# Optimization experiments

Hardware: AMD Instinct MI355X
Metric: run time of the kernel (lower is better)

## Reference

```python
import jax, jax.numpy as jnp
import numpy as np

N_NODES = 100000
N_EDGES = 1600000
HEADS = 8
CH = 16
NEG_SLOPE = 0.2


def setup_inputs() -> dict:
    key = jax.random.key(0)
    ks = jax.random.split(key, 8)
    x = jax.random.normal(ks[0], (N_NODES, 16), dtype=jnp.float32)
    edge_index = jax.random.randint(ks[1], (2, N_EDGES), 0, N_NODES, dtype=jnp.int64)
    W = jax.random.normal(ks[2], (16, HEADS * CH), dtype=jnp.float32) * 0.25
    att_src = jax.random.normal(ks[3], (HEADS, CH), dtype=jnp.float32) * 0.25
    att_dst = jax.random.normal(ks[4], (HEADS, CH), dtype=jnp.float32) * 0.25
    bias = jax.random.normal(ks[5], (HEADS * CH,), dtype=jnp.float32) * 0.1
    fc_w = jax.random.normal(ks[6], (HEADS * CH, 5), dtype=jnp.float32) * 0.1
    fc_b = jax.random.normal(ks[7], (5,), dtype=jnp.float32) * 0.1
    return {"x": x, "edge_index": edge_index, "W": W, "att_src": att_src,
            "att_dst": att_dst, "bias": bias, "fc_w": fc_w, "fc_b": fc_b}


def reference(x, edge_index, W, att_src, att_dst, bias, fc_w, fc_b):
    N = x.shape[0]
    # PyG GATConv default: add self loops
    loops = jnp.arange(N, dtype=edge_index.dtype)
    src = jnp.concatenate([edge_index[0], loops])
    dst = jnp.concatenate([edge_index[1], loops])

    h = (x @ W).reshape(N, HEADS, CH)                 # [N,H,C]
    a_src = jnp.einsum('nhc,hc->nh', h, att_src)      # [N,H]
    a_dst = jnp.einsum('nhc,hc->nh', h, att_dst)      # [N,H]

    e = a_src[src] + a_dst[dst]                       # [E,H]
    e = jax.nn.leaky_relu(e, NEG_SLOPE)
    # segment softmax over edges grouped by destination node
    e_max = jax.ops.segment_max(e, dst, num_segments=N)
    e_exp = jnp.exp(e - e_max[dst])
    denom = jax.ops.segment_sum(e_exp, dst, num_segments=N)
    alpha = e_exp / (denom[dst] + 1e-16)              # [E,H]

    msg = alpha[:, :, None] * h[src]                  # [E,H,C]
    out = jax.ops.segment_sum(msg, dst, num_segments=N)  # [N,H,C]
    out = out.reshape(N, HEADS * CH) + bias           # concat heads + bias

    out = jax.nn.relu(out)
    # dropout is identity in eval mode
    logits = out @ fc_w + fc_b                        # [N,5]
    return jax.nn.log_softmax(logits, axis=1)
```

## Files before the change

kernel.cpp:

```cpp
#include <hip/hip_runtime.h>
#include <hip/hip_bf16.h>
#include <hip/hip_fp16.h>
#include <math.h>

#define N_NODES 100000
#define N_EDGES 1600000
#define HEADS 8
#define HC 128
#define LOG2E 1.44269504f

#define DPB 64
#define NB 1563
#define NBP (NB + 1)
#define NCH 512
#define EPC (N_EDGES / NCH)
#define CAPS 1664
#define WSTR (CAPS + 4)
#define NA 196

__global__ __launch_bounds__(512) void k_prep(
    const float* __restrict__ x, const float* __restrict__ W,
    const float* __restrict__ att_s, const float* __restrict__ att_d,
    const int* __restrict__ ei,
    unsigned short* __restrict__ a_srcb, float* __restrict__ a_dst,
    uint4* __restrict__ x2b,
    int* __restrict__ offs, unsigned* __restrict__ stg) {
    __shared__ int smem[2048 + EPC];
    __shared__ int ws8[8];
    int t = threadIdx.x;
    if (blockIdx.x >= NCH) {
        float* sM = (float*)smem;
        if (t < 256) {
            int k = t >> 4, h2 = t & 15;
            const float* av = (h2 < 8) ? att_s : att_d;
            int h = h2 & 7;
            float s = 0.f;
#pragma unroll
            for (int c = 0; c < 16; ++c)
                s = fmaf(W[k * HC + h * 16 + c], av[h * 16 + c], s);
            sM[k * 16 + h2] = s * LOG2E;
        }
        __syncthreads();
        int node = (blockIdx.x - NCH) * 512 + t;
        if (node < N_NODES) {
            const float4* xr = (const float4*)(x + node * 16);
            float4 x0 = xr[0], x1 = xr[1], x2 = xr[2], x3 = xr[3];
            float xv[16] = {x0.x, x0.y, x0.z, x0.w, x1.x, x1.y, x1.z, x1.w,
                            x2.x, x2.y, x2.z, x2.w, x3.x, x3.y, x3.z, x3.w};
            union { uint4 u[2]; __hip_bfloat162 b[8]; } px;
#pragma unroll
            for (int k = 0; k < 8; ++k)
                px.b[k] = __float22bfloat162_rn(float2{xv[2 * k], xv[2 * k + 1]});
            x2b[node * 2] = px.u[0];
            x2b[node * 2 + 1] = px.u[1];
            float oo[16];
#pragma unroll
            for (int h2 = 0; h2 < 16; ++h2) {
                float o = 0.f;
#pragma unroll
                for (int k = 0; k < 16; ++k) o = fmaf(xv[k], sM[k * 16 + h2], o);
                oo[h2] = o;
            }
            union { uint4 u; unsigned short s[8]; } pb;
#pragma unroll
            for (int h = 0; h < 8; ++h)
                pb.s[h] = __bfloat16_as_ushort(__float2bfloat16(oo[h]));
            *(uint4*)(a_srcb + (size_t)node * 8) = pb.u;
            float4 d0 = {oo[8], oo[9], oo[10], oo[11]};
            float4 d1 = {oo[12], oo[13], oo[14], oo[15]};
            *(float4*)(a_dst + (size_t)node * 8) = d0;
            *(float4*)(a_dst + (size_t)node * 8 + 4) = d1;
        }
    } else {
        int* hist = smem;
        unsigned* entries = (unsigned*)(smem + 2048);
        int c = blockIdx.x;
        hist[t] = 0; hist[t + 512] = 0; hist[t + 1024] = 0; hist[t + 1536] = 0;
        __syncthreads();
        int beg = c * EPC, end = beg + EPC;
        for (int e = beg + t; e < end; e += 512)
            atomicAdd(&hist[ei[N_EDGES + e] >> 6], 1);
        __syncthreads();
        int i0 = 4 * t;
        int v0 = hist[i0], v1 = hist[i0 + 1], v2 = hist[i0 + 2], v3 = hist[i0 + 3];
        int s1 = v0 + v1, s2 = s1 + v2, T = s2 + v3;
        int lane = t & 63, wv = t >> 6;
        int inc = T;
#pragma unroll
        for (int off = 1; off < 64; off <<= 1) {
            int y = __shfl_up(inc, off);
            if (lane >= off) inc += y;
        }
        if (lane == 63) ws8[wv] = inc;
        __syncthreads();
        int wbase = 0;
        for (int k = 0; k < wv; ++k) wbase += ws8[k];
        int e0 = wbase + inc - T;
        hist[i0] = e0; hist[i0 + 1] = e0 + v0;
        hist[i0 + 2] = e0 + s1; hist[i0 + 3] = e0 + s2;
        __syncthreads();
        int row = c * NBP;
        for (int b = t; b < NB; b += 512) offs[row + b] = hist[b];
        if (t == 0) offs[row + NB] = EPC;
        __syncthreads();
        for (int e = beg + t; e < end; e += 512) {
            int src = ei[e], dst = ei[N_EDGES + e];
            int pos = atomicAdd(&hist[dst >> 6], 1);
            entries[pos] = ((unsigned)(dst & 63) << 17) | (unsigned)src;
        }
        __syncthreads();
        unsigned* so = stg + beg;
        for (int i = t; i < EPC; i += 512) so[i] = entries[i];
    }
}

__global__ __launch_bounds__(256) void k_tr(const int* __restrict__ offs,
                                            int* __restrict__ offsT) {
    __shared__ int tile[64][65];
    int b0 = (blockIdx.x >> 3) * 64;
    int c0 = (blockIdx.x & 7) * 64;
    int t = threadIdx.x;
    for (int i = t; i < 4096; i += 256) {
        int cc = i >> 6, bb = i & 63;
        int b = b0 + bb;
        tile[bb][cc] = (b < NBP) ? offs[(c0 + cc) * NBP + b] : 0;
    }
    __syncthreads();
    for (int i = t; i < 4096; i += 256) {
        int bb = i >> 6, cc = i & 63;
        int b = b0 + bb;
        if (b < NBP) offsT[b * NCH + c0 + cc] = tile[bb][cc];
    }
}

__global__ __launch_bounds__(512) void k_gather(
    const __hip_bfloat162* __restrict__ x2b,
    const unsigned short* __restrict__ a_srcb, const float* __restrict__ W,
    const float* __restrict__ a_dst,
    const int* __restrict__ offsT, const unsigned* __restrict__ stg,
    const float* __restrict__ bias, const float* __restrict__ fc_w,
    const float* __restrict__ fc_b, float* __restrict__ out) {
    __shared__ __align__(16) unsigned buf0[(8 * WSTR) / 2];
    __shared__ __align__(16) int sbuf[CAPS];
    __shared__ __align__(16) float sW[16 * HC];
    __shared__ __align__(16) float sad[8 * DPB + 8];
    __shared__ int hist[DPB];
    __shared__ int bs[DPB + 1];
    __shared__ int rord[DPB];
    __shared__ int ws8[8];
    unsigned* estage = buf0;
    unsigned short* wst = (unsigned short*)buf0;
    int* cstage = sbuf;
    int* o0_s = sbuf;
    int* myb_s = sbuf + 512;
    int b = blockIdx.x, t = threadIdx.x;
    int d0 = b * DPB;
    for (int i = t; i < 16 * HC; i += 512) {
        int c = i & 127, k = i >> 7;
        int blk = c >> 3;
        int sb = blk ^ ((blk >> 2) & 3);
        sW[k * HC + sb * 8 + (c & 7)] = W[i];
    }
    sad[t] = (d0 * 8 + t < N_NODES * 8) ? a_dst[(size_t)d0 * 8 + t] : 0.f;
    if (t < 8) sad[8 * DPB + t] = -100000.f;
    int lane = t & 63, wv = t >> 6;
    {
        int o0 = offsT[b * NCH + t];
        int len = offsT[(b + 1) * NCH + t] - o0;
        o0_s[t] = o0;
        int inc = len;
#pragma unroll
        for (int off = 1; off < 64; off <<= 1) {
            int y = __shfl_up(inc, off);
            if (lane >= off) inc += y;
        }
        if (lane == 63) ws8[wv] = inc;
        __syncthreads();
        int wbase = 0;
        for (int k = 0; k < wv; ++k) wbase += ws8[k];
        myb_s[t] = wbase + inc - len;
        if (t == 511) myb_s[NCH] = wbase + inc;
    }
    if (t < DPB) hist[t] = (d0 + t < N_NODES) ? 1 : 0;
    __syncthreads();
    int tot = myb_s[NCH];
    for (int i = t; i < tot; i += 512) {
        int lo = 0, hi = NCH - 1;
#pragma unroll
        for (int s = 0; s < 9; ++s) {
            int mid = (lo + hi + 1) >> 1;
            if (myb_s[mid] <= i) lo = mid; else hi = mid - 1;
        }
        estage[i] = stg[lo * EPC + o0_s[lo] + (i - myb_s[lo])];
    }
    __syncthreads();
    for (int i = t; i < tot; i += 512) atomicAdd(&hist[estage[i] >> 17], 1);
    __syncthreads();
    if (t < 64) {
        int gd = d0 + t;
        bool val = gd < N_NODES;
        int len = hist[t];
        int plen = (len + 3) & ~3;
        int iv = plen;
#pragma unroll
        for (int off = 1; off < 64; off <<= 1) {
            int y = __shfl_up(iv, off);
            if (t >= off) iv += y;
        }
        int excl = iv - plen;
        bs[t] = excl;
        if (t == 63) bs[64] = iv;
        if (val) cstage[excl] = (t << 17) | gd;
        hist[t] = excl + (val ? 1 : 0);
        for (int k = len; k < plen; ++k) cstage[excl + k] = (64 << 17);
        int key = (plen << 6) | t;
#pragma unroll
        for (int k = 2; k <= 64; k <<= 1) {
#pragma unroll
            for (int jj = k >> 1; jj >= 1; jj >>= 1) {
                int partner = __shfl_xor(key, jj);
                bool up = ((t & k) == 0);
                bool takeMax = (((t & jj) != 0) == up);
                key = takeMax ? (key > partner ? key : partner)
                              : (key < partner ? key : partner);
            }
        }
        rord[t] = key & 63;
    }
    __syncthreads();
    for (int i = t; i < tot; i += 512) {
        unsigned u = estage[i];
        int pos = atomicAdd(&hist[u >> 17], 1);
        cstage[pos] = (int)u;
    }
    __syncthreads();
    int ctot = bs[DPB];
    for (int i = t; i < ctot; i += 512) {
        unsigned u = (unsigned)cstage[i];
        int s = (int)(u & 0x1FFFF);
        int dl = (int)(u >> 17);
        union { uint4 v; __hip_bfloat162 b2[4]; } pa;
        pa.v = *(const uint4*)(a_srcb + (size_t)s * 8);
        const float* adp = sad + dl * 8;
        float4 ad0 = *(const float4*)(adp);
        float4 ad1 = *(const float4*)(adp + 4);
        float2 s01 = __bfloat1622float2(pa.b2[0]);
        float2 s23 = __bfloat1622float2(pa.b2[1]);
        float2 s45 = __bfloat1622float2(pa.b2[2]);
        float2 s67 = __bfloat1622float2(pa.b2[3]);
        float e[8] = {s01.x + ad0.x, s01.y + ad0.y, s23.x + ad0.z, s23.y + ad0.w,
                      s45.x + ad1.x, s45.y + ad1.y, s67.x + ad1.z, s67.y + ad1.w};
#pragma unroll
        for (int h = 0; h < 8; ++h) {
            float eh = fmaxf(e[h], 0.2f * e[h]);
            float w = exp2f(eh);
            wst[h * WSTR + i] = __half_as_ushort(__float2half(w));
        }
    }
    __syncthreads();
    int q = t & 15, g = t >> 4;
    int head = q >> 1, i8 = q & 1;
    int c0 = head * 16 + i8 * 8;
    int blk0 = c0 >> 3;
    int sw0 = (blk0 ^ ((blk0 >> 2) & 3)) * 8;
    const unsigned short* wrow = wst + head * WSTR;
    int xofs = i8 * 16;
    const char* xb = (const char*)x2b;
    float bb[8], fwv[8][5], fbv[5];
#pragma unroll
    for (int m = 0; m < 8; ++m) bb[m] = bias[c0 + m];
#pragma unroll
    for (int m = 0; m < 8; ++m)
#pragma unroll
        for (int jj = 0; jj < 5; ++jj) fwv[m][jj] = fc_w[(c0 + m) * 5 + jj];
#pragma unroll
    for (int jj = 0; jj < 5; ++jj) fbv[jj] = fc_b[jj];
    for (int l4 = 0; l4 < 2; ++l4) {
        int l = rord[l4 == 0 ? g : 63 - g];
        int gd = d0 + l;
        if (gd >= N_NODES) continue;
        int beg = bs[l], end = bs[l + 1];
        float A[8] = {0.f, 0.f, 0.f, 0.f, 0.f, 0.f, 0.f, 0.f};
        float wsum = 0.f;
        auto acc = [&](const uint4& xv, float w) {
            union { uint4 v; __hip_bfloat162 b2[4]; } xx; xx.v = xv;
            float2 f0 = __bfloat1622float2(xx.b2[0]);
            float2 f1 = __bfloat1622float2(xx.b2[1]);
            float2 f2 = __bfloat1622float2(xx.b2[2]);
            float2 f3 = __bfloat1622float2(xx.b2[3]);
            A[0] = fmaf(w, f0.x, A[0]); A[1] = fmaf(w, f0.y, A[1]);
            A[2] = fmaf(w, f1.x, A[2]); A[3] = fmaf(w, f1.y, A[3]);
            A[4] = fmaf(w, f2.x, A[4]); A[5] = fmaf(w, f2.y, A[5]);
            A[6] = fmaf(w, f3.x, A[6]); A[7] = fmaf(w, f3.y, A[7]);
        };
        for (int j = beg; j < end; j += 4) {
            int4 cs = *(const int4*)(cstage + j);
            uint2 wu = *(const uint2*)(wrow + j);
            union { uint2 u2; __half2 h2[2]; } wq; wq.u2 = wu;
            float2 w01 = __half22float2(wq.h2[0]);
            float2 w23 = __half22float2(wq.h2[1]);
            int s0 = cs.x & 0x1FFFF, s1 = cs.y & 0x1FFFF;
            int s2 = cs.z & 0x1FFFF, s3 = cs.w & 0x1FFFF;
            uint4 xv0 = *(const uint4*)(xb + ((s0 << 5) + xofs));
            uint4 xv1 = *(const uint4*)(xb + ((s1 << 5) + xofs));
            uint4 xv2 = *(const uint4*)(xb + ((s2 << 5) + xofs));
            uint4 xv3 = *(const uint4*)(xb + ((s3 << 5) + xofs));
            acc(xv0, w01.x); acc(xv1, w01.y);
            acc(xv2, w23.x); acc(xv3, w23.y);
            wsum += (w01.x + w01.y) + (w23.x + w23.y);
        }
        float inv = 1.f / (wsum + 1e-16f);
#pragma unroll
        for (int m = 0; m < 8; ++m) A[m] *= inv;
        float ov[8] = {0.f, 0.f, 0.f, 0.f, 0.f, 0.f, 0.f, 0.f};
#pragma unroll
        for (int m = 0; m < 8; ++m) {
            float a = A[m];
            float ap = __shfl_xor(A[m], 1);
            const float* w0r = sW + (i8 * 8 + m) * HC + sw0;
            const float* w1r = sW + ((1 - i8) * 8 + m) * HC + sw0;
#pragma unroll
            for (int o = 0; o < 8; ++o) ov[o] = fmaf(a, w0r[o], ov[o]);
#pragma unroll
            for (int o = 0; o < 8; ++o) ov[o] = fmaf(ap, w1r[o], ov[o]);
        }
#pragma unroll
        for (int m = 0; m < 8; ++m) ov[m] = fmaxf(ov[m] + bb[m], 0.f);
        float p[5];
#pragma unroll
        for (int jj = 0; jj < 5; ++jj) {
            float sacc = 0.f;
#pragma unroll
            for (int m = 0; m < 8; ++m) sacc = fmaf(ov[m], fwv[m][jj], sacc);
            p[jj] = sacc;
        }
#pragma unroll
        for (int off = 8; off >= 1; off >>= 1)
#pragma unroll
            for (int jj = 0; jj < 5; ++jj) p[jj] += __shfl_xor(p[jj], off);
        if (q == 0) {
            float lg[5], mx = -1e30f;
#pragma unroll
            for (int jj = 0; jj < 5; ++jj) {
                lg[jj] = p[jj] + fbv[jj];
                mx = fmaxf(mx, lg[jj]);
            }
            float sum = 0.f;
#pragma unroll
            for (int jj = 0; jj < 5; ++jj) sum += __expf(lg[jj] - mx);
            float ls = mx + __logf(sum);
#pragma unroll
            for (int jj = 0; jj < 5; ++jj) out[gd * 5 + jj] = lg[jj] - ls;
        }
    }
}

extern "C" void kernel_launch(void* const* d_in, const int* in_sizes, int n_in,
                              void* d_out, int out_size, void* d_ws, size_t ws_size,
                              hipStream_t stream) {
    const float* x     = (const float*)d_in[0];
    const int*   ei    = (const int*)d_in[1];
    const float* W     = (const float*)d_in[2];
    const float* att_s = (const float*)d_in[3];
    const float* att_d = (const float*)d_in[4];
    const float* bias  = (const float*)d_in[5];
    const float* fc_w  = (const float*)d_in[6];
    const float* fc_b  = (const float*)d_in[7];
    float* out = (float*)d_out;

    char* ws = (char*)d_ws;
    size_t off = 0;
    auto carve = [&](size_t bytes) {
        void* p = ws + off;
        off = (off + bytes + 255) & ~(size_t)255;
        return p;
    };
    unsigned short* a_srcb = (unsigned short*)carve((size_t)N_NODES * HEADS * 2);
    float*    a_dst = (float*)   carve((size_t)N_NODES * HEADS * 4);
    uint4*    x2b   = (uint4*)   carve((size_t)N_NODES * 32);
    int*      offs  = (int*)     carve((size_t)NCH * NBP * 4);
    int*      offsT = (int*)     carve((size_t)NBP * NCH * 4);
    unsigned* stg   = (unsigned*)carve((size_t)N_EDGES * 4);

    k_prep<<<NCH + NA, 512, 0, stream>>>(x, W, att_s, att_d, ei,
                                         a_srcb, a_dst, x2b, offs, stg);
    k_tr<<<200, 256, 0, stream>>>(offs, offsT);
    k_gather<<<NB, 512, 0, stream>>>((const __hip_bfloat162*)x2b, a_srcb, W,
                                     a_dst, offsT, stg, bias, fc_w, fc_b, out);
}
```

Baseline: 169.2 us.

## Split prep kernel, fuse histogram into staging loop, drop bitonic row ordering

The combined prep kernel is split into a counting-sort kernel and a separate per-node attention-projection kernel launched with 256-thread blocks. In the gather kernel, the destination histogram is now counted in the same loop that stages edges, which removes one pass and one barrier. The bitonic sort that ordered destination rows by length for load balancing is removed, and rows are assigned to groups in a fixed interleaved order. This trades possible load imbalance across row groups for less setup work, and adds one extra kernel launch.

```diff
diff --git a/kernel.cpp b/kernel.cpp
--- a/kernel.cpp
+++ b/kernel.cpp
@@ -16,101 +16,102 @@
 #define EPC (N_EDGES / NCH)
 #define CAPS 1664
 #define WSTR (CAPS + 4)
-#define NA 196
-
-__global__ __launch_bounds__(512) void k_prep(
+#define NAB 391
+
+__global__ __launch_bounds__(512) void k_csort(
+    const int* __restrict__ ei, int* __restrict__ offs,
+    unsigned* __restrict__ stg) {
+    __shared__ int hist[2048];
+    __shared__ int entries_s[EPC];
+    __shared__ int ws8[8];
+    unsigned* entries = (unsigned*)entries_s;
+    int t = threadIdx.x;
+    int c = blockIdx.x;
+    hist[t] = 0; hist[t + 512] = 0; hist[t + 1024] = 0; hist[t + 1536] = 0;
+    __syncthreads();
+    int beg = c * EPC, end = beg + EPC;
+    for (int e = beg + t; e < end; e += 512)
+        atomicAdd(&hist[ei[N_EDGES + e] >> 6], 1);
+    __syncthreads();
+    int i0 = 4 * t;
+    int v0 = hist[i0], v1 = hist[i0 + 1], v2 = hist[i0 + 2], v3 = hist[i0 + 3];
+    int s1 = v0 + v1, s2 = s1 + v2, T = s2 + v3;
+    int lane = t & 63, wv = t >> 6;
+    int inc = T;
+#pragma unroll
+    for (int off = 1; off < 64; off <<= 1) {
+        int y = __shfl_up(inc, off);
+        if (lane >= off) inc += y;
+    }
+    if (lane == 63) ws8[wv] = inc;
+    __syncthreads();
+    int wbase = 0;
+    for (int k = 0; k < wv; ++k) wbase += ws8[k];
+    int e0 = wbase + inc - T;
+    hist[i0] = e0; hist[i0 + 1] = e0 + v0;
+    hist[i0 + 2] = e0 + s1; hist[i0 + 3] = e0 + s2;
+    __syncthreads();
+    int row = c * NBP;
+    for (int b = t; b < NB; b += 512) offs[row + b] = hist[b];
+    if (t == 0) offs[row + NB] = EPC;
+    __syncthreads();
+    for (int e = beg + t; e < end; e += 512) {
+        int src = ei[e], dst = ei[N_EDGES + e];
+        int pos = atomicAdd(&hist[dst >> 6], 1);
+        entries[pos] = ((unsigned)(dst & 63) << 17) | (unsigned)src;
+    }
+    __syncthreads();
+    unsigned* so = stg + beg;
+    for (int i = t; i < EPC; i += 512) so[i] = entries[i];
+}
+
+__global__ __launch_bounds__(256) void k_amat(
     const float* __restrict__ x, const float* __restrict__ W,
     const float* __restrict__ att_s, const float* __restrict__ att_d,
-    const int* __restrict__ ei,
     unsigned short* __restrict__ a_srcb, float* __restrict__ a_dst,
-    uint4* __restrict__ x2b,
-    int* __restrict__ offs, unsigned* __restrict__ stg) {
-    __shared__ int smem[2048 + EPC];
-    __shared__ int ws8[8];
+    uint4* __restrict__ x2b) {
+    __shared__ float sM[256];
     int t = threadIdx.x;
-    if (blockIdx.x >= NCH) {
-        float* sM = (float*)smem;
-        if (t < 256) {
-            int k = t >> 4, h2 = t & 15;
-            const float* av = (h2 < 8) ? att_s : att_d;
-            int h = h2 & 7;
-            float s = 0.f;
-#pragma unroll
-            for (int c = 0; c < 16; ++c)
-                s = fmaf(W[k * HC + h * 16 + c], av[h * 16 + c], s);
-            sM[k * 16 + h2] = s * LOG2E;
-        }
-        __syncthreads();
-        int node = (blockIdx.x - NCH) * 512 + t;
-        if (node < N_NODES) {
-            const float4* xr = (const float4*)(x + node * 16);
-            float4 x0 = xr[0], x1 = xr[1], x2 = xr[2], x3 = xr[3];
-            float xv[16] = {x0.x, x0.y, x0.z, x0.w, x1.x, x1.y, x1.z, x1.w,
-                            x2.x, x2.y, x2.z, x2.w, x3.x, x3.y, x3.z, x3.w};
-            union { uint4 u[2]; __hip_bfloat162 b[8]; } px;
-#pragma unroll
-            for (int k = 0; k < 8; ++k)
-                px.b[k] = __float22bfloat162_rn(float2{xv[2 * k], xv[2 * k + 1]});
-            x2b[node * 2] = px.u[0];
-            x2b[node * 2 + 1] = px.u[1];
-            float oo[16];
-#pragma unroll
-            for (int h2 = 0; h2 < 16; ++h2) {
-                float o = 0.f;
-#pragma unroll
-                for (int k = 0; k < 16; ++k) o = fmaf(xv[k], sM[k * 16 + h2], o);
-                oo[h2] = o;
-            }
-            union { uint4 u; unsigned short s[8]; } pb;
-#pragma unroll
-            for (int h = 0; h < 8; ++h)
-                pb.s[h] = __bfloat16_as_ushort(__float2bfloat16(oo[h]));
-            *(uint4*)(a_srcb + (size_t)node * 8) = pb.u;
-            float4 d0 = {oo[8], oo[9], oo[10], oo[11]};
-            float4 d1 = {oo[12], oo[13], oo[14], oo[15]};
-            *(float4*)(a_dst + (size_t)node * 8) = d0;
-            *(float4*)(a_dst + (size_t)node * 8 + 4) = d1;
-        }
-    } else {
-        int* hist = smem;
-        unsigned* entries = (unsigned*)(smem + 2048);
-        int c = blockIdx.x;
-        hist[t] = 0; hist[t + 512] = 0; hist[t + 1024] = 0; hist[t + 1536] = 0;
-        __syncthreads();
-        int beg = c * EPC, end = beg + EPC;
-        for (int e = beg + t; e < end; e += 512)
-            atomicAdd(&hist[ei[N_EDGES + e] >> 6], 1);
-        __syncthreads();
-        int i0 = 4 * t;
-        int v0 = hist[i0], v1 = hist[i0 + 1], v2 = hist[i0 + 2], v3 = hist[i0 + 3];
-        int s1 = v0 + v1, s2 = s1 + v2, T = s2 + v3;
-        int lane = t & 63, wv = t >> 6;
-        int inc = T;
-#pragma unroll
-        for (int off = 1; off < 64; off <<= 1) {
-            int y = __shfl_up(inc, off);
-            if (lane >= off) inc += y;
-        }
-        if (lane == 63) ws8[wv] = inc;
-        __syncthreads();
-        int wbase = 0;
-        for (int k = 0; k < wv; ++k) wbase += ws8[k];
-        int e0 = wbase + inc - T;
-        hist[i0] = e0; hist[i0 + 1] = e0 + v0;
-        hist[i0 + 2] = e0 + s1; hist[i0 + 3] = e0 + s2;
-        __syncthreads();
-        int row = c * NBP;
-        for (int b = t; b < NB; b += 512) offs[row + b] = hist[b];
-        if (t == 0) offs[row + NB] = EPC;
-        __syncthreads();
-        for (int e = beg + t; e < end; e += 512) {
-            int src = ei[e], dst = ei[N_EDGES + e];
-            int pos = atomicAdd(&hist[dst >> 6], 1);
-            entries[pos] = ((unsigned)(dst & 63) << 17) | (unsigned)src;
-        }
-        __syncthreads();
-        unsigned* so = stg + beg;
-        for (int i = t; i < EPC; i += 512) so[i] = entries[i];
+    {
+        int k = t >> 4, h2 = t & 15;
+        const float* av = (h2 < 8) ? att_s : att_d;
+        int h = h2 & 7;
+        float s = 0.f;
+#pragma unroll
+        for (int c = 0; c < 16; ++c)
+            s = fmaf(W[k * HC + h * 16 + c], av[h * 16 + c], s);
+        sM[k * 16 + h2] = s * LOG2E;
+    }
+    __syncthreads();
+    int node = blockIdx.x * 256 + t;
+    if (node < N_NODES) {
+        const float4* xr = (const float4*)(x + node * 16);
+        float4 x0 = xr[0], x1 = xr[1], x2 = xr[2], x3 = xr[3];
+        float xv[16] = {x0.x, x0.y, x0.z, x0.w, x1.x, x1.y, x1.z, x1.w,
+                        x2.x, x2.y, x2.z, x2.w, x3.x, x3.y, x3.z, x3.w};
+        union { uint4 u[2]; __hip_bfloat162 b[8]; } px;
+#pragma unroll
+        for (int k = 0; k < 8; ++k)
+            px.b[k] = __float22bfloat162_rn(float2{xv[2 * k], xv[2 * k + 1]});
+        x2b[node * 2] = px.u[0];
+        x2b[node * 2 + 1] = px.u[1];
+        float oo[16];
+#pragma unroll
+        for (int h2 = 0; h2 < 16; ++h2) {
+            float o = 0.f;
+#pragma unroll
+            for (int k = 0; k < 16; ++k) o = fmaf(xv[k], sM[k * 16 + h2], o);
+            oo[h2] = o;
+        }
+        union { uint4 u; unsigned short s[8]; } pb;
+#pragma unroll
+        for (int h = 0; h < 8; ++h)
+            pb.s[h] = __bfloat16_as_ushort(__float2bfloat16(oo[h]));
+        *(uint4*)(a_srcb + (size_t)node * 8) = pb.u;
+        float4 d0 = {oo[8], oo[9], oo[10], oo[11]};
+        float4 d1 = {oo[12], oo[13], oo[14], oo[15]};
+        *(float4*)(a_dst + (size_t)node * 8) = d0;
+        *(float4*)(a_dst + (size_t)node * 8 + 4) = d1;
     }
 }
 
@@ -146,7 +147,6 @@
     __shared__ __align__(16) float sad[8 * DPB + 8];
     __shared__ int hist[DPB];
     __shared__ int bs[DPB + 1];
-    __shared__ int rord[DPB];
     __shared__ int ws8[8];
     unsigned* estage = buf0;
     unsigned short* wst = (unsigned short*)buf0;
@@ -191,10 +191,10 @@
             int mid = (lo + hi + 1) >> 1;
             if (myb_s[mid] <= i) lo = mid; else hi = mid - 1;
         }
-        estage[i] = stg[lo * EPC + o0_s[lo] + (i - myb_s[lo])];
-    }
-    __syncthreads();
-    for (int i = t; i < tot; i += 512) atomicAdd(&hist[estage[i] >> 17], 1);
+        unsigned u = stg[lo * EPC + o0_s[lo] + (i - myb_s[lo])];
+        estage[i] = u;
+        atomicAdd(&hist[u >> 17], 1);
+    }
     __syncthreads();
     if (t < 64) {
         int gd = d0 + t;
@@ -213,19 +213,6 @@
         if (val) cstage[excl] = (t << 17) | gd;
         hist[t] = excl + (val ? 1 : 0);
         for (int k = len; k < plen; ++k) cstage[excl + k] = (64 << 17);
-        int key = (plen << 6) | t;
-#pragma unroll
-        for (int k = 2; k <= 64; k <<= 1) {
-#pragma unroll
-            for (int jj = k >> 1; jj >= 1; jj >>= 1) {
-                int partner = __shfl_xor(key, jj);
-                bool up = ((t & k) == 0);
-                bool takeMax = (((t & jj) != 0) == up);
-                key = takeMax ? (key > partner ? key : partner)
-                              : (key < partner ? key : partner);
-            }
-        }
-        rord[t] = key & 63;
     }
     __syncthreads();
     for (int i = t; i < tot; i += 512) {
@@ -276,9 +263,9 @@
 #pragma unroll
     for (int jj = 0; jj < 5; ++jj) fbv[jj] = fc_b[jj];
     for (int l4 = 0; l4 < 2; ++l4) {
-        int l = rord[l4 == 0 ? g : 63 - g];
+        int l = g * 2 + l4;
         int gd = d0 + l;
-        if (gd >= N_NODES) continue;
+        if (gd >= N_NODES) break;
         int beg = bs[l], end = bs[l + 1];
         float A[8] = {0.f, 0.f, 0.f, 0.f, 0.f, 0.f, 0.f, 0.f};
         float wsum = 0.f;
@@ -382,8 +369,8 @@
     int*      offsT = (int*)     carve((size_t)NBP * NCH * 4);
     unsigned* stg   = (unsigned*)carve((size_t)N_EDGES * 4);
 
-    k_prep<<<NCH + NA, 512, 0, stream>>>(x, W, att_s, att_d, ei,
-                                         a_srcb, a_dst, x2b, offs, stg);
+    k_csort<<<NCH, 512, 0, stream>>>(ei, offs, stg);
+    k_amat<<<NAB, 256, 0, stream>>>(x, W, att_s, att_d, a_srcb, a_dst, x2b);
     k_tr<<<200, 256, 0, stream>>>(offs, offsT);
     k_gather<<<NB, 512, 0, stream>>>((const __hip_bfloat162*)x2b, a_srcb, W,
                                      a_dst, offsT, stg, bias, fc_w, fc_b, out);
```

New measurement: 169.8 us. No clear change (+0.3%).
